# Performance work log

Measured on AMD Instinct MI355X. Metric: run time of the kernel, lower is better.

Reference implementation:

```python
import jax, jax.numpy as jnp
import numpy as np

DIM = 192
K = 3
RED = 4
B, H, W = 4, 256, 256
EPS = 1e-5  # BatchNorm eps

def _make_mask():
    # PixelCNN mask type 'A': zero the center pixel and everything after it
    m = np.ones((DIM, 1, K, K), np.float32)
    m[:, :, K // 2, K // 2:] = 0.0  # center row: center col onward
    m[:, :, K // 2 + 1:] = 0.0      # all rows below center
    return jnp.asarray(m)

MASK = _make_mask()  # [DIM, 1, K, K]

def setup_inputs() -> dict:
    key = jax.random.key(0)
    ks = jax.random.split(key, 4)
    r = DIM // RED
    return {
        "x": jax.random.normal(ks[0], (B, DIM, H, W), jnp.float32),
        "w1": jax.random.normal(ks[1], (r, DIM), jnp.float32) * 0.05,      # conv1 1x1, no bias
        "gamma": jnp.ones((r,), jnp.float32),                               # BN weight
        "beta": jnp.zeros((r,), jnp.float32),                               # BN bias
        "running_mean": jnp.zeros((r,), jnp.float32),
        "running_var": jnp.ones((r,), jnp.float32),
        "w2": jax.random.normal(ks[2], (DIM * K * K, r), jnp.float32) * 0.05,  # conv2 1x1
        "b2": jnp.zeros((DIM * K * K,), jnp.float32),
        "bias": jnp.zeros((DIM,), jnp.float32),                             # depthwise conv bias
    }

def reference(x, w1, gamma, beta, running_mean, running_var, w2, b2, bias):
    b, c, h, w = x.shape  # c == DIM
    # --- dynamic weight generation: pool -> 1x1 conv -> BN(eval) -> ReLU -> 1x1 conv ---
    pooled = x.mean(axis=(2, 3))                                   # [b, dim]
    t = pooled @ w1.T                                              # [b, dim//red]
    t = gamma * (t - running_mean) * jax.lax.rsqrt(running_var + EPS) + beta
    t = jax.nn.relu(t)
    wt = t @ w2.T + b2                                             # [b, dim*K*K]
    wt = wt.reshape(b * DIM, 1, K, K) * jnp.tile(MASK, (b, 1, 1, 1))
    # --- per-sample masked depthwise conv via batch-folding (groups = b*dim) ---
    out = jax.lax.conv_general_dilated(
        x.reshape(1, b * c, h, w), wt,
        window_strides=(1, 1), padding=((1, 1), (1, 1)),
        feature_group_count=b * DIM,
        dimension_numbers=("NCHW", "OIHW", "NCHW"))                # [1, b*dim, h, w]
    out = out + jnp.tile(bias, (b,))[None, :, None, None]
    return out.reshape(b, c, h, w)
```

## Files before the change

kernel.cpp:

```cpp
#include <hip/hip_runtime.h>

#define DIMC 192
#define HID  48
#define HW   65536
#define WIDTH 256
#define NPLANE 768

typedef float nfloat4 __attribute__((ext_vector_type(4)));


__global__ __launch_bounds__(256) void k_pool_s(const float* __restrict__ xs,
                                                float* __restrict__ pp) {
    const int plane = blockIdx.x >> 2;
    const int strip = blockIdx.x & 3;
    const float4* p = (const float4*)(xs + (size_t)plane * HW + strip * 64 * WIDTH);
    const int t = threadIdx.x;
    float s = 0.f;
#pragma unroll
    for (int k = 0; k < 16; ++k) {
        float4 v = p[k * 256 + t];
        s += (v.x + v.y) + (v.z + v.w);
    }
#pragma unroll
    for (int off = 32; off > 0; off >>= 1) s += __shfl_down(s, off, 64);
    __shared__ float wsum[4];
    const int wave = t >> 6, lane = t & 63;
    if (lane == 0) wsum[wave] = s;
    __syncthreads();
    if (t == 0) pp[blockIdx.x] = (wsum[0] + wsum[1]) + (wsum[2] + wsum[3]);
}

__global__ __launch_bounds__(256) void k_conv_s(
    const float* __restrict__ xs,
    const float* __restrict__ pp,
    const float* __restrict__ w1,
    const float* __restrict__ gamma,
    const float* __restrict__ beta,
    const float* __restrict__ rmean,
    const float* __restrict__ rvar,
    const float* __restrict__ w2,
    const float* __restrict__ b2,
    const float* __restrict__ bias,
    float* __restrict__ outs)
{
    const int c = blockIdx.x >> 3;
    const int tid = threadIdx.x;

    __shared__ float P[DIMC];
    __shared__ float T[HID];
    __shared__ float W4[4];
    if (tid < DIMC) {
        float4 v = ((const float4*)pp)[tid];
        P[tid] = ((v.x + v.y) + (v.z + v.w)) * (1.0f / 65536.0f);
    }
    __syncthreads();
    {
        const int g = tid >> 2, l = tid & 3;
        if (g < HID) {
            const float* wr = w1 + g * DIMC;
            float acc = 0.f;
#pragma unroll 8
            for (int d = l; d < DIMC; d += 4) acc += P[d] * wr[d];
            acc += __shfl_xor(acc, 1, 64);
            acc += __shfl_xor(acc, 2, 64);
            if (l == 0) {
                const float inv = rsqrtf(rvar[g] + 1e-5f);
                float v = gamma[g] * (acc - rmean[g]) * inv + beta[g];
                T[g] = v > 0.f ? v : 0.f;
            }
        }
        __syncthreads();
        if (tid < 4) {
            const int o = c * 9 + tid;
            const float* wr = w2 + o * HID;
            float acc = b2[o];
#pragma unroll
            for (int j = 0; j < HID; ++j) acc += T[j] * wr[j];
            W4[tid] = acc;
        }
        __syncthreads();
    }
    const float4 wt = make_float4(W4[0], W4[1], W4[2], W4[3]);
    const float bs = bias[c];

    const int wave = tid >> 6;
    const int lane = tid & 63;
    const int y0 = ((blockIdx.x & 7) << 5) + (wave << 3);
    const float4* xp = (const float4*)(xs + (size_t)c * HW);
    nfloat4* op = (nfloat4*)(outs + (size_t)c * HW);

    float4 a;
    if (y0 == 0) a = make_float4(0.f, 0.f, 0.f, 0.f);
    else         a = xp[(y0 - 1) * 64 + lane];

#pragma unroll
    for (int r = 0; r < 8; ++r) {
        const int y = y0 + r;
        float4 bb = xp[y * 64 + lane];
        float leftA  = __shfl_up(a.w, 1, 64);   if (lane == 0)  leftA  = 0.f;
        float rightA = __shfl_down(a.x, 1, 64); if (lane == 63) rightA = 0.f;
        float leftB  = __shfl_up(bb.w, 1, 64);  if (lane == 0)  leftB  = 0.f;
        nfloat4 o;
        o.x = wt.x * leftA + wt.y * a.x + wt.z * a.y    + wt.w * leftB + bs;
        o.y = wt.x * a.x   + wt.y * a.y + wt.z * a.z    + wt.w * bb.x  + bs;
        o.z = wt.x * a.y   + wt.y * a.z + wt.z * a.w    + wt.w * bb.y  + bs;
        o.w = wt.x * a.z   + wt.y * a.w + wt.z * rightA + wt.w * bb.z  + bs;
        __builtin_nontemporal_store(o, &op[y * 64 + lane]);
        a = bb;
    }
}

extern "C" void kernel_launch(void* const* d_in, const int* in_sizes, int n_in,
                              void* d_out, int out_size, void* d_ws, size_t ws_size,
                              hipStream_t stream) {
    const float* x     = (const float*)d_in[0];
    const float* w1    = (const float*)d_in[1];
    const float* gamma = (const float*)d_in[2];
    const float* beta  = (const float*)d_in[3];
    const float* rmean = (const float*)d_in[4];
    const float* rvar  = (const float*)d_in[5];
    const float* w2    = (const float*)d_in[6];
    const float* b2    = (const float*)d_in[7];
    const float* bias  = (const float*)d_in[8];
    float* out = (float*)d_out;

    float* pp = (float*)d_ws;

    for (int b = 0; b < 4; ++b) {
        const float* xs = x   + (size_t)b * DIMC * HW;
        float* outs     = out + (size_t)b * DIMC * HW;
        k_pool_s<<<768, 256, 0, stream>>>(xs, pp + b * 768);
        k_conv_s<<<1536, 256, 0, stream>>>(xs, pp + b * 768, w1, gamma, beta,
                                           rmean, rvar, w2, b2, bias, outs);
    }
}
```

Baseline: 410.9 us.

## Merge per-batch launches and prefetch conv rows before weight generation

Replaces the four per-batch pool/conv launch pairs with one pool and one conv launch over all planes. The conv kernel issues all its row loads, including scalar halo loads in place of shuffles, before the dynamic-weight MLP, so memory latency overlaps the small matmuls. Output stores become normal stores instead of nontemporal ones. The cost is more registers per thread, extra scalar halo loads, and the loss of per-batch cache locality between the pool and conv passes, since x (~200MB) is now re-read after the whole tensor has streamed.

```diff
diff --git a/kernel.cpp b/kernel.cpp
--- a/kernel.cpp
+++ b/kernel.cpp
@@ -6,14 +6,11 @@
 #define WIDTH 256
 #define NPLANE 768
 
-typedef float nfloat4 __attribute__((ext_vector_type(4)));
-
-
-__global__ __launch_bounds__(256) void k_pool_s(const float* __restrict__ xs,
-                                                float* __restrict__ pp) {
+__global__ __launch_bounds__(256) void k_pool(const float* __restrict__ x,
+                                              float* __restrict__ pp) {
     const int plane = blockIdx.x >> 2;
     const int strip = blockIdx.x & 3;
-    const float4* p = (const float4*)(xs + (size_t)plane * HW + strip * 64 * WIDTH);
+    const float4* p = (const float4*)(x + (size_t)plane * HW + strip * 64 * WIDTH);
     const int t = threadIdx.x;
     float s = 0.f;
 #pragma unroll
@@ -30,8 +27,8 @@
     if (t == 0) pp[blockIdx.x] = (wsum[0] + wsum[1]) + (wsum[2] + wsum[3]);
 }
 
-__global__ __launch_bounds__(256) void k_conv_s(
-    const float* __restrict__ xs,
+__global__ __launch_bounds__(256) void k_conv(
+    const float* __restrict__ x,
     const float* __restrict__ pp,
     const float* __restrict__ w1,
     const float* __restrict__ gamma,
@@ -41,16 +38,42 @@
     const float* __restrict__ w2,
     const float* __restrict__ b2,
     const float* __restrict__ bias,
-    float* __restrict__ outs)
+    float* __restrict__ out)
 {
-    const int c = blockIdx.x >> 3;
+    const int plane = blockIdx.x >> 3;
+    const int b = plane / DIMC;
+    const int c = plane - b * DIMC;
     const int tid = threadIdx.x;
+    const int wave = tid >> 6;
+    const int lane = tid & 63;
+    const int y0 = ((blockIdx.x & 7) << 5) + (wave << 3);
+    const int x0 = lane << 2;
+
+    const float*  xs  = x + (size_t)plane * HW;
+    const float4* xp4 = (const float4*)xs;
+
+    float4 R[9];
+    float  LA[9];
+    float  RA[8];
+#pragma unroll
+    for (int r = 0; r < 9; ++r) {
+        const int y = y0 - 1 + r;
+        if (y < 0) {
+            R[r] = make_float4(0.f, 0.f, 0.f, 0.f);
+            LA[r] = 0.f;
+            if (r < 8) RA[r] = 0.f;
+        } else {
+            R[r] = xp4[y * 64 + lane];
+            LA[r] = (lane == 0)  ? 0.f : xs[y * WIDTH + x0 - 1];
+            if (r < 8) RA[r] = (lane == 63) ? 0.f : xs[y * WIDTH + x0 + 4];
+        }
+    }
 
     __shared__ float P[DIMC];
     __shared__ float T[HID];
     __shared__ float W4[4];
     if (tid < DIMC) {
-        float4 v = ((const float4*)pp)[tid];
+        float4 v = ((const float4*)pp)[b * DIMC + tid];
         P[tid] = ((v.x + v.y) + (v.z + v.w)) * (1.0f / 65536.0f);
     }
     __syncthreads();
@@ -83,30 +106,15 @@
     const float4 wt = make_float4(W4[0], W4[1], W4[2], W4[3]);
     const float bs = bias[c];
 
-    const int wave = tid >> 6;
-    const int lane = tid & 63;
-    const int y0 = ((blockIdx.x & 7) << 5) + (wave << 3);
-    const float4* xp = (const float4*)(xs + (size_t)c * HW);
-    nfloat4* op = (nfloat4*)(outs + (size_t)c * HW);
-
-    float4 a;
-    if (y0 == 0) a = make_float4(0.f, 0.f, 0.f, 0.f);
-    else         a = xp[(y0 - 1) * 64 + lane];
-
+    float4* op = (float4*)(out + (size_t)plane * HW);
 #pragma unroll
     for (int r = 0; r < 8; ++r) {
-        const int y = y0 + r;
-        float4 bb = xp[y * 64 + lane];
-        float leftA  = __shfl_up(a.w, 1, 64);   if (lane == 0)  leftA  = 0.f;
-        float rightA = __shfl_down(a.x, 1, 64); if (lane == 63) rightA = 0.f;
-        float leftB  = __shfl_up(bb.w, 1, 64);  if (lane == 0)  leftB  = 0.f;
-        nfloat4 o;
-        o.x = wt.x * leftA + wt.y * a.x + wt.z * a.y    + wt.w * leftB + bs;
-        o.y = wt.x * a.x   + wt.y * a.y + wt.z * a.z    + wt.w * bb.x  + bs;
-        o.z = wt.x * a.y   + wt.y * a.z + wt.z * a.w    + wt.w * bb.y  + bs;
-        o.w = wt.x * a.z   + wt.y * a.w + wt.z * rightA + wt.w * bb.z  + bs;
-        __builtin_nontemporal_store(o, &op[y * 64 + lane]);
-        a = bb;
+        float4 o;
+        o.x = wt.x * LA[r]   + wt.y * R[r].x + wt.z * R[r].y + wt.w * LA[r+1]   + bs;
+        o.y = wt.x * R[r].x  + wt.y * R[r].y + wt.z * R[r].z + wt.w * R[r+1].x  + bs;
+        o.z = wt.x * R[r].y  + wt.y * R[r].z + wt.z * R[r].w + wt.w * R[r+1].y  + bs;
+        o.w = wt.x * R[r].z  + wt.y * R[r].w + wt.z * RA[r]  + wt.w * R[r+1].z  + bs;
+        op[(y0 + r) * 64 + lane] = o;
     }
 }
 
@@ -126,11 +134,7 @@
 
     float* pp = (float*)d_ws;
 
-    for (int b = 0; b < 4; ++b) {
-        const float* xs = x   + (size_t)b * DIMC * HW;
-        float* outs     = out + (size_t)b * DIMC * HW;
-        k_pool_s<<<768, 256, 0, stream>>>(xs, pp + b * 768);
-        k_conv_s<<<1536, 256, 0, stream>>>(xs, pp + b * 768, w1, gamma, beta,
-                                           rmean, rvar, w2, b2, bias, outs);
-    }
+    k_pool<<<NPLANE * 4, 256, 0, stream>>>(x, pp);
+    k_conv<<<NPLANE * 8, 256, 0, stream>>>(x, pp, w1, gamma, beta,
+                                           rmean, rvar, w2, b2, bias, out);
 }
```

Measured after the change: 421.5 us. 2.6% more time.

## Fuse pooling and depthwise conv into one cooperative kernel with on-chip plane reuse

Applied to the files above, without the earlier changes.

Replaces the per-batch pool and conv kernel pairs with one cooperative kernel. Each block reads its quarter-plane once, keeps it in registers and LDS, contributes partial sums, waits on a grid-wide sync, then computes the dynamic weights and the masked convolution from the on-chip copy. This removes the second global read of x and the extra launches. In exchange it adds four grid syncs, heavy LDS use (48 KB per block) that limits occupancy, and drops the nontemporal stores. A two-kernel fallback runs if the cooperative launch fails.

```diff
diff --git a/kernel.cpp b/kernel.cpp
--- a/kernel.cpp
+++ b/kernel.cpp
@@ -1,4 +1,7 @@
 #include <hip/hip_runtime.h>
+#include <hip/hip_cooperative_groups.h>
+
+namespace cg = cooperative_groups;
 
 #define DIMC 192
 #define HID  48
@@ -6,33 +9,9 @@
 #define WIDTH 256
 #define NPLANE 768
 
-typedef float nfloat4 __attribute__((ext_vector_type(4)));
-
-
-__global__ __launch_bounds__(256) void k_pool_s(const float* __restrict__ xs,
-                                                float* __restrict__ pp) {
-    const int plane = blockIdx.x >> 2;
-    const int strip = blockIdx.x & 3;
-    const float4* p = (const float4*)(xs + (size_t)plane * HW + strip * 64 * WIDTH);
-    const int t = threadIdx.x;
-    float s = 0.f;
-#pragma unroll
-    for (int k = 0; k < 16; ++k) {
-        float4 v = p[k * 256 + t];
-        s += (v.x + v.y) + (v.z + v.w);
-    }
-#pragma unroll
-    for (int off = 32; off > 0; off >>= 1) s += __shfl_down(s, off, 64);
-    __shared__ float wsum[4];
-    const int wave = t >> 6, lane = t & 63;
-    if (lane == 0) wsum[wave] = s;
-    __syncthreads();
-    if (t == 0) pp[blockIdx.x] = (wsum[0] + wsum[1]) + (wsum[2] + wsum[3]);
-}
-
-__global__ __launch_bounds__(256) void k_conv_s(
-    const float* __restrict__ xs,
-    const float* __restrict__ pp,
+__global__ __launch_bounds__(256, 3) void k_fused(
+    const float* __restrict__ x,
+    float* __restrict__ pp,
     const float* __restrict__ w1,
     const float* __restrict__ gamma,
     const float* __restrict__ beta,
@@ -41,16 +20,147 @@
     const float* __restrict__ w2,
     const float* __restrict__ b2,
     const float* __restrict__ bias,
-    float* __restrict__ outs)
+    float* __restrict__ out)
 {
-    const int c = blockIdx.x >> 3;
-    const int tid = threadIdx.x;
-
+    const int c     = blockIdx.x >> 2;
+    const int chunk = blockIdx.x & 3;
+    const int r0    = chunk << 6;
+    const int tid   = threadIdx.x;
+    const int wave  = tid >> 6;
+    const int lane  = tid & 63;
+
+    __shared__ float4 XT[48 * 64];
     __shared__ float P[DIMC];
     __shared__ float T[HID];
-    __shared__ float W4[4];
+    __shared__ float W4v[4];
+    __shared__ float wsum[4];
+
+    float4 R[4];
+
+    for (int b = 0; b < 4; ++b) {
+        const int plane = b * DIMC + c;
+        const float4* xp4 = (const float4*)(x + (size_t)plane * HW);
+
+        float s = 0.f;
+#pragma unroll
+        for (int j = 0; j < 4; ++j) {
+            R[j] = xp4[(r0 + wave * 16 + j) * 64 + lane];
+            s += (R[j].x + R[j].y) + (R[j].z + R[j].w);
+        }
+#pragma unroll
+        for (int j = 0; j < 12; ++j) {
+            float4 v = xp4[(r0 + wave * 16 + 4 + j) * 64 + lane];
+            XT[(wave * 12 + j) * 64 + lane] = v;
+            s += (v.x + v.y) + (v.z + v.w);
+        }
+#pragma unroll
+        for (int off = 32; off > 0; off >>= 1) s += __shfl_down(s, off, 64);
+        if (lane == 0) wsum[wave] = s;
+        __syncthreads();
+        if (tid == 0) {
+            pp[plane * 4 + chunk] = (wsum[0] + wsum[1]) + (wsum[2] + wsum[3]);
+            __threadfence();
+        }
+        cg::this_grid().sync();
+
+        if (tid < DIMC) {
+            float4 v = ((const float4*)pp)[b * DIMC + tid];
+            P[tid] = ((v.x + v.y) + (v.z + v.w)) * (1.0f / 65536.0f);
+        }
+        __syncthreads();
+        {
+            const int g = tid >> 2, l = tid & 3;
+            if (g < HID) {
+                const float* wr = w1 + g * DIMC;
+                float acc = 0.f;
+#pragma unroll 8
+                for (int d = l; d < DIMC; d += 4) acc += P[d] * wr[d];
+                acc += __shfl_xor(acc, 1, 64);
+                acc += __shfl_xor(acc, 2, 64);
+                if (l == 0) {
+                    const float inv = rsqrtf(rvar[g] + 1e-5f);
+                    float v = gamma[g] * (acc - rmean[g]) * inv + beta[g];
+                    T[g] = v > 0.f ? v : 0.f;
+                }
+            }
+            __syncthreads();
+            if (tid < 4) {
+                const int o = c * 9 + tid;
+                const float* wr = w2 + o * HID;
+                float acc = b2[o];
+#pragma unroll
+                for (int j = 0; j < HID; ++j) acc += T[j] * wr[j];
+                W4v[tid] = acc;
+            }
+            __syncthreads();
+        }
+        const float4 wt = make_float4(W4v[0], W4v[1], W4v[2], W4v[3]);
+        const float bs = bias[c];
+
+        float4* op = (float4*)(out + (size_t)plane * HW);
+        float4 a;
+        {
+            const int gy = r0 + wave * 16 - 1;
+            if (gy < 0)          a = make_float4(0.f, 0.f, 0.f, 0.f);
+            else if (wave == 0)  a = xp4[gy * 64 + lane];
+            else                 a = XT[(wave * 12 - 1) * 64 + lane];
+        }
+#pragma unroll
+        for (int rr = 0; rr < 16; ++rr) {
+            float4 bb = (rr < 4) ? R[rr] : XT[(wave * 12 + (rr - 4)) * 64 + lane];
+            float leftA  = __shfl_up(a.w, 1, 64);   if (lane == 0)  leftA  = 0.f;
+            float rightA = __shfl_down(a.x, 1, 64); if (lane == 63) rightA = 0.f;
+            float leftB  = __shfl_up(bb.w, 1, 64);  if (lane == 0)  leftB  = 0.f;
+            float4 o;
+            o.x = wt.x * leftA + wt.y * a.x + wt.z * a.y    + wt.w * leftB + bs;
+            o.y = wt.x * a.x   + wt.y * a.y + wt.z * a.z    + wt.w * bb.x  + bs;
+            o.z = wt.x * a.y   + wt.y * a.z + wt.z * a.w    + wt.w * bb.y  + bs;
+            o.w = wt.x * a.z   + wt.y * a.w + wt.z * rightA + wt.w * bb.z  + bs;
+            op[(r0 + wave * 16 + rr) * 64 + lane] = o;
+            a = bb;
+        }
+        __syncthreads();
+    }
+}
+
+__global__ __launch_bounds__(256) void k_pool_fb(const float* __restrict__ x,
+                                                 float* __restrict__ pp) {
+    const int plane = blockIdx.x >> 2;
+    const int strip = blockIdx.x & 3;
+    const float4* p = (const float4*)(x + (size_t)plane * HW + strip * 64 * WIDTH);
+    const int t = threadIdx.x;
+    float s = 0.f;
+#pragma unroll
+    for (int k = 0; k < 16; ++k) {
+        float4 v = p[k * 256 + t];
+        s += (v.x + v.y) + (v.z + v.w);
+    }
+#pragma unroll
+    for (int off = 32; off > 0; off >>= 1) s += __shfl_down(s, off, 64);
+    __shared__ float wsum[4];
+    const int wave = t >> 6, lane = t & 63;
+    if (lane == 0) wsum[wave] = s;
+    __syncthreads();
+    if (t == 0) pp[blockIdx.x] = (wsum[0] + wsum[1]) + (wsum[2] + wsum[3]);
+}
+
+__global__ __launch_bounds__(256) void k_conv_fb(
+    const float* __restrict__ x, const float* __restrict__ pp,
+    const float* __restrict__ w1, const float* __restrict__ gamma,
+    const float* __restrict__ beta, const float* __restrict__ rmean,
+    const float* __restrict__ rvar, const float* __restrict__ w2,
+    const float* __restrict__ b2, const float* __restrict__ bias,
+    float* __restrict__ out)
+{
+    const int plane = blockIdx.x >> 3;
+    const int b = plane / DIMC;
+    const int c = plane - b * DIMC;
+    const int tid = threadIdx.x;
+    __shared__ float P[DIMC];
+    __shared__ float T[HID];
+    __shared__ float W4v[4];
     if (tid < DIMC) {
-        float4 v = ((const float4*)pp)[tid];
+        float4 v = ((const float4*)pp)[b * DIMC + tid];
         P[tid] = ((v.x + v.y) + (v.z + v.w)) * (1.0f / 65536.0f);
     }
     __syncthreads();
@@ -76,23 +186,19 @@
             float acc = b2[o];
 #pragma unroll
             for (int j = 0; j < HID; ++j) acc += T[j] * wr[j];
-            W4[tid] = acc;
-        }
-        __syncthreads();
-    }
-    const float4 wt = make_float4(W4[0], W4[1], W4[2], W4[3]);
+            W4v[tid] = acc;
+        }
+        __syncthreads();
+    }
+    const float4 wt = make_float4(W4v[0], W4v[1], W4v[2], W4v[3]);
     const float bs = bias[c];
-
-    const int wave = tid >> 6;
-    const int lane = tid & 63;
+    const int wave = tid >> 6, lane = tid & 63;
     const int y0 = ((blockIdx.x & 7) << 5) + (wave << 3);
-    const float4* xp = (const float4*)(xs + (size_t)c * HW);
-    nfloat4* op = (nfloat4*)(outs + (size_t)c * HW);
-
+    const float4* xp = (const float4*)(x + (size_t)plane * HW);
+    float4* op = (float4*)(out + (size_t)plane * HW);
     float4 a;
     if (y0 == 0) a = make_float4(0.f, 0.f, 0.f, 0.f);
     else         a = xp[(y0 - 1) * 64 + lane];
-
 #pragma unroll
     for (int r = 0; r < 8; ++r) {
         const int y = y0 + r;
@@ -100,12 +206,12 @@
         float leftA  = __shfl_up(a.w, 1, 64);   if (lane == 0)  leftA  = 0.f;
         float rightA = __shfl_down(a.x, 1, 64); if (lane == 63) rightA = 0.f;
         float leftB  = __shfl_up(bb.w, 1, 64);  if (lane == 0)  leftB  = 0.f;
-        nfloat4 o;
+        float4 o;
         o.x = wt.x * leftA + wt.y * a.x + wt.z * a.y    + wt.w * leftB + bs;
         o.y = wt.x * a.x   + wt.y * a.y + wt.z * a.z    + wt.w * bb.x  + bs;
         o.z = wt.x * a.y   + wt.y * a.z + wt.z * a.w    + wt.w * bb.y  + bs;
         o.w = wt.x * a.z   + wt.y * a.w + wt.z * rightA + wt.w * bb.z  + bs;
-        __builtin_nontemporal_store(o, &op[y * 64 + lane]);
+        op[y * 64 + lane] = o;
         a = bb;
     }
 }
@@ -126,11 +232,15 @@
 
     float* pp = (float*)d_ws;
 
-    for (int b = 0; b < 4; ++b) {
-        const float* xs = x   + (size_t)b * DIMC * HW;
-        float* outs     = out + (size_t)b * DIMC * HW;
-        k_pool_s<<<768, 256, 0, stream>>>(xs, pp + b * 768);
-        k_conv_s<<<1536, 256, 0, stream>>>(xs, pp + b * 768, w1, gamma, beta,
-                                           rmean, rvar, w2, b2, bias, outs);
-    }
-}
+    void* args[] = {(void*)&x, (void*)&pp, (void*)&w1, (void*)&gamma,
+                    (void*)&beta, (void*)&rmean, (void*)&rvar, (void*)&w2,
+                    (void*)&b2, (void*)&bias, (void*)&out};
+    hipError_t err = hipLaunchCooperativeKernel((const void*)k_fused,
+                                                dim3(NPLANE), dim3(256),
+                                                args, 0, stream);
+    if (err != hipSuccess) {
+        k_pool_fb<<<NPLANE * 4, 256, 0, stream>>>(x, pp);
+        k_conv_fb<<<NPLANE * 8, 256, 0, stream>>>(x, pp, w1, gamma, beta,
+                                                  rmean, rvar, w2, b2, bias, out);
+    }
+}
```

After: 867.4 us. 111% more time.
